# Kernel tuning notes

Hardware: AMD Instinct MI355X
Metric: run time of the kernel (lower is better)

## Reference

```python
import jax, jax.numpy as jnp
import numpy as np

N = 30000          # num nodes
E = 480000         # num edges (avg degree 16)
IN = 1024          # in_channels
OUT = 128          # out_channels
MAX_DEG = 48       # static cap on per-node in-degree (incl. self-loop); Poisson(16) max over 30k nodes << 48


def setup_inputs() -> dict:
    key = jax.random.key(0)
    k1, k2, k3 = jax.random.split(key, 3)
    x = jax.random.normal(k1, (N, IN), dtype=jnp.float32)
    edge_index = jax.random.randint(k2, (2, E), 0, N, dtype=jnp.int64)
    W = jax.random.normal(k3, (IN, OUT), dtype=jnp.float32) * (1.0 / np.sqrt(IN))
    b = jnp.zeros((OUT,), dtype=jnp.float32)
    return {"x": x, "edge_index": edge_index, "W": W, "b": b}


def _median_conv(x, edge_index, W, b):
    # linear transform first (as in the torch module)
    h = x @ W                                   # [N, OUT]
    n = x.shape[0]
    # add self-loops
    loop = jnp.arange(n, dtype=edge_index.dtype)
    row = jnp.concatenate([edge_index[0], loop])  # source nodes
    col = jnp.concatenate([edge_index[1], loop])  # destination nodes
    # sort edges by destination (jnp.argsort is stable)
    order = jnp.argsort(col)
    row_s = row[order]
    col_s = col[order]
    x_j = h[row_s]                              # [Etot, OUT] gathered neighbor features
    # per-destination degree and within-segment slot index
    ones = jnp.ones_like(col_s)
    deg = jax.ops.segment_sum(ones, col_s, num_segments=n)      # [N]
    start = jnp.cumsum(deg) - deg                                # segment start offsets
    slot = jnp.arange(col_s.shape[0], dtype=col_s.dtype) - start[col_s]
    # padded dense batch [N, MAX_DEG, OUT]; pads = +inf so they sort to the end
    dense = jnp.full((n, MAX_DEG, h.shape[1]), jnp.inf, dtype=h.dtype)
    dense = dense.at[col_s, slot].set(x_j)
    sdense = jnp.sort(dense, axis=1)
    # torch.median returns the LOWER median: sorted index (deg-1)//2
    med_idx = jnp.maximum(deg - 1, 0) // 2                       # [N]
    out = jnp.take_along_axis(sdense, med_idx[:, None, None], axis=1)[:, 0, :]
    # zero-degree nodes would yield +inf; self-loops guarantee deg>=1, but guard anyway
    out = jnp.where((deg > 0)[:, None], out, jnp.zeros_like(out))
    return out + b


def reference(x, edge_index, W, b):
    return _median_conv(x, edge_index, W, b)
```

## Files before the change

kernel.cpp:

```cpp
#include <hip/hip_runtime.h>
#include <hip/hip_bf16.h>

#define N_NODES 30000
#define N_EDGES 480000
#define IN_CH   1024
#define OUT_CH  128
#define MAX_DEG 48

#define BM 64
#define BK 64
#define NSTEP (IN_CH / BK)

typedef float   f32x4  __attribute__((ext_vector_type(4)));
typedef __bf16  bf16x8 __attribute__((ext_vector_type(8)));
typedef unsigned short ushort8 __attribute__((ext_vector_type(8)));
typedef unsigned int   uint4v  __attribute__((ext_vector_type(4)));

__device__ __forceinline__ unsigned short f2bf(float f) {
  unsigned int u = __builtin_bit_cast(unsigned int, f);
  u += 0x7fffu + ((u >> 16) & 1u);
  return (unsigned short)(u >> 16);
}

__device__ __forceinline__ unsigned int cvt_pk(float lo, float hi) {
  unsigned int r;
  asm("v_cvt_pk_bf16_f32 %0, %1, %2" : "=v"(r) : "v"(lo), "v"(hi));
  return r;
}

__device__ __forceinline__ void gload_lds16(const void* g, void* l) {
  __builtin_amdgcn_global_load_lds(
      (const __attribute__((address_space(1))) void*)g,
      (__attribute__((address_space(3))) void*)l, 16, 0, 0);
}

__global__ __launch_bounds__(256) void convert_W(const float* __restrict__ W,
                                                 unsigned short* __restrict__ Wt) {
  int idx = blockIdx.x * 256 + threadIdx.x;
  int n = idx >> 10;
  int k = idx & 1023;
  Wt[idx] = f2bf(W[k * OUT_CH + n]);
}

__global__ __launch_bounds__(256) void build_adj(const int* __restrict__ ei,
                                                 int* __restrict__ deg,
                                                 int* __restrict__ adj) {
  int i = blockIdx.x * blockDim.x + threadIdx.x;
  const int total = N_EDGES + N_NODES;
  if (i >= total) return;
  int src, dst;
  if (i < N_EDGES) { src = ei[i]; dst = ei[N_EDGES + i]; }
  else             { src = i - N_EDGES; dst = src; }
  int slot = atomicAdd(&deg[dst], 1);
  if (slot < MAX_DEG) adj[dst * MAX_DEG + slot] = src;
}

__global__ __launch_bounds__(256) void gemm_h(const float* __restrict__ x,
                                              const unsigned short* __restrict__ Wt,
                                              const float* __restrict__ bias,
                                              float* __restrict__ h) {
  __shared__ char smem[2 * 32768];
  const int tid  = threadIdx.x;
  const int wv   = tid >> 6;
  const int lane = tid & 63;
  const int l16  = lane & 15;
  const int g4   = lane >> 4;
  const int m0   = blockIdx.x * BM;

  f32x4 acc[4][2];
#pragma unroll
  for (int rf = 0; rf < 4; ++rf)
#pragma unroll
    for (int cf = 0; cf < 2; ++cf) acc[rf][cf] = (f32x4){0.f, 0.f, 0.f, 0.f};

  auto stage = [&](int buf, int st) {
    const int k0 = st * BK;
    char* sA = smem + buf * 32768;
    char* sB = sA + 16384;
#pragma unroll
    for (int j = 0; j < 4; ++j) {
      const int blk = wv * 4 + j;
      const int rowA = blk * 4 + (lane >> 4);
      int rg = m0 + rowA;
      if (rg > N_NODES - 1) rg = N_NODES - 1;
      const float* srcA = x + (size_t)rg * IN_CH + k0
                        + (((lane & 15) ^ (rowA & 15)) << 2);
      gload_lds16(srcA, sA + blk * 1024 + lane * 16);
      const int c = blk * 8 + (lane >> 3);
      const unsigned short* srcB = Wt + (size_t)c * IN_CH + k0
                                 + (((lane & 7) ^ (c & 7)) << 3);
      gload_lds16(srcB, sB + blk * 1024 + lane * 16);
    }
  };

  auto compute = [&](int buf) {
    const char* sA = smem + buf * 32768;
    const char* sB = sA + 16384;
#pragma unroll
    for (int ks = 0; ks < 2; ++ks) {
      bf16x8 bfr[2];
#pragma unroll
      for (int cf = 0; cf < 2; ++cf) {
        const int c = wv * 32 + cf * 16 + l16;
        const int slot = (ks * 4 + g4) ^ (c & 7);
        bfr[cf] = *(const bf16x8*)(sB + c * 128 + slot * 16);
      }
#pragma unroll
      for (int rf = 0; rf < 4; ++rf) {
        const int row = rf * 16 + l16;
        const int q0 = ((ks * 8 + g4 * 2) ^ (row & 15)) << 4;
        const int q1 = ((ks * 8 + g4 * 2 + 1) ^ (row & 15)) << 4;
        f32x4 a0 = *(const f32x4*)(sA + row * 256 + q0);
        f32x4 a1 = *(const f32x4*)(sA + row * 256 + q1);
        uint4v aw;
        aw[0] = cvt_pk(a0[0], a0[1]);
        aw[1] = cvt_pk(a0[2], a0[3]);
        aw[2] = cvt_pk(a1[0], a1[1]);
        aw[3] = cvt_pk(a1[2], a1[3]);
        bf16x8 av = __builtin_bit_cast(bf16x8, aw);
        acc[rf][0] = __builtin_amdgcn_mfma_f32_16x16x32_bf16(av, bfr[0], acc[rf][0], 0, 0, 0);
        acc[rf][1] = __builtin_amdgcn_mfma_f32_16x16x32_bf16(av, bfr[1], acc[rf][1], 0, 0, 0);
      }
    }
  };

  stage(0, 0);
  __syncthreads();
  int cur = 0;
  for (int st = 0; st < NSTEP - 1; ++st) {
    stage(cur ^ 1, st + 1);
    compute(cur);
    __syncthreads();
    cur ^= 1;
  }
  compute(cur);

  const int crow0 = m0 + g4 * 4;
#pragma unroll
  for (int cf = 0; cf < 2; ++cf) {
    const int col = wv * 32 + cf * 16 + l16;
    const float bv = bias[col];
#pragma unroll
    for (int rf = 0; rf < 4; ++rf) {
#pragma unroll
      for (int i = 0; i < 4; ++i) {
        int r = crow0 + rf * 16 + i;
        if (r < N_NODES) h[(size_t)r * OUT_CH + col] = acc[rf][cf][i] + bv;
      }
    }
  }
}

template <int NS>
__device__ __forceinline__ void batcher_sort(float (&a)[NS]) {
#pragma unroll
  for (int p = 1; p < NS; p <<= 1) {
#pragma unroll
    for (int k = p; k >= 1; k >>= 1) {
#pragma unroll
      for (int j = k % p; j + k < NS; j += 2 * k) {
#pragma unroll
        for (int i = 0; i < k; ++i) {
          if (i + j + k < NS) {
            if ((i + j) / (2 * p) == (i + j + k) / (2 * p)) {
              float lo = fminf(a[i + j], a[i + j + k]);
              float hi = fmaxf(a[i + j], a[i + j + k]);
              a[i + j] = lo;
              a[i + j + k] = hi;
            }
          }
        }
      }
    }
  }
}

template <int NS>
__device__ __forceinline__ float med_n(const float* __restrict__ h,
                                       const int* nbrs, int d, int m, int ch) {
  float a[NS];
#pragma unroll
  for (int j = 0; j < NS; ++j) {
    if (j < d) a[j] = h[(size_t)nbrs[j] * OUT_CH + ch];
    else       a[j] = 1e30f;
  }
  batcher_sort<NS>(a);
  float med = a[0];
#pragma unroll
  for (int j = 1; j < NS; ++j) med = (j == m) ? a[j] : med;
  return med;
}

__global__ __launch_bounds__(128) void median_kernel(const float* __restrict__ h,
                                                     const int* __restrict__ adj,
                                                     const int* __restrict__ deg,
                                                     float* __restrict__ out) {
  __shared__ int nbrs[64];
  const int node = blockIdx.x;
  const int ch   = threadIdx.x;
  int d = deg[node];
  if (d > MAX_DEG) d = MAX_DEG;
  if (ch < 64) nbrs[ch] = (ch < d && ch < MAX_DEG) ? adj[node * MAX_DEG + ch] : 0;
  __syncthreads();
  const int m = (d - 1) >> 1;

  float med;
  if (d <= 8)       med = med_n<8>(h, nbrs, d, m, ch);
  else if (d <= 16) med = med_n<16>(h, nbrs, d, m, ch);
  else if (d <= 32) med = med_n<32>(h, nbrs, d, m, ch);
  else              med = med_n<64>(h, nbrs, d, m, ch);

  out[(size_t)node * OUT_CH + ch] = med;
}

extern "C" void kernel_launch(void* const* d_in, const int* in_sizes, int n_in,
                              void* d_out, int out_size, void* d_ws, size_t ws_size,
                              hipStream_t stream) {
  const float* x  = (const float*)d_in[0];
  const int*   ei = (const int*)d_in[1];
  const float* W  = (const float*)d_in[2];
  const float* b  = (const float*)d_in[3];
  float* out = (float*)d_out;

  char* ws = (char*)d_ws;
  float*          h   = (float*)ws;
  unsigned short* Wt  = (unsigned short*)(ws + 15360000);
  int*            deg = (int*)(ws + 15360000 + 262144);
  int*            adj = (int*)(ws + 15360000 + 262144 + 120000);

  hipMemsetAsync(deg, 0, N_NODES * sizeof(int), stream);
  convert_W<<<dim3(131072 / 256), dim3(256), 0, stream>>>(W, Wt);
  build_adj<<<dim3((N_EDGES + N_NODES + 255) / 256), dim3(256), 0, stream>>>(ei, deg, adj);
  gemm_h<<<dim3((N_NODES + BM - 1) / BM), dim3(256), 0, stream>>>(x, Wt, b, h);
  median_kernel<<<dim3(N_NODES), dim3(128), 0, stream>>>(h, adj, deg, out);
}
```

Baseline: 273.9 us.

## Store h as fp16 and sort two channels per lane with packed f16 min/max

```diff
diff --git a/kernel.cpp b/kernel.cpp
--- a/kernel.cpp
+++ b/kernel.cpp
@@ -7,11 +7,12 @@
 #define OUT_CH  128
 #define MAX_DEG 48
 
-#define BM 64
+#define BM 32
 #define BK 64
 #define NSTEP (IN_CH / BK)
 
 typedef float   f32x4  __attribute__((ext_vector_type(4)));
+typedef float   f32x2  __attribute__((ext_vector_type(2)));
 typedef __bf16  bf16x8 __attribute__((ext_vector_type(8)));
 typedef unsigned short ushort8 __attribute__((ext_vector_type(8)));
 typedef unsigned int   uint4v  __attribute__((ext_vector_type(4)));
@@ -28,6 +29,20 @@
   return r;
 }
 
+__device__ __forceinline__ unsigned pk_min(unsigned a, unsigned b) {
+  unsigned r; asm("v_pk_min_f16 %0, %1, %2" : "=v"(r) : "v"(a), "v"(b)); return r;
+}
+__device__ __forceinline__ unsigned pk_max(unsigned a, unsigned b) {
+  unsigned r; asm("v_pk_max_f16 %0, %1, %2" : "=v"(r) : "v"(a), "v"(b)); return r;
+}
+__device__ __forceinline__ float f16_to_f32(unsigned u16) {
+  float f; asm("v_cvt_f32_f16 %0, %1" : "=v"(f) : "v"(u16)); return f;
+}
+__device__ __forceinline__ unsigned short f32_to_f16(float f) {
+  unsigned r; asm("v_cvt_f16_f32 %0, %1" : "=v"(r) : "v"(f));
+  return (unsigned short)(r & 0xffffu);
+}
+
 __device__ __forceinline__ void gload_lds16(const void* g, void* l) {
   __builtin_amdgcn_global_load_lds(
       (const __attribute__((address_space(1))) void*)g,
@@ -35,11 +50,26 @@
 }
 
 __global__ __launch_bounds__(256) void convert_W(const float* __restrict__ W,
-                                                 unsigned short* __restrict__ Wt) {
-  int idx = blockIdx.x * 256 + threadIdx.x;
-  int n = idx >> 10;
-  int k = idx & 1023;
-  Wt[idx] = f2bf(W[k * OUT_CH + n]);
+                                                 unsigned short* __restrict__ Wtt) {
+  __shared__ float tile[64][132];
+  const int tid = threadIdx.x;
+  const int k0  = blockIdx.x * 64;
+#pragma unroll
+  for (int it = 0; it < 32; ++it) {
+    int id = it * 256 + tid;
+    int kk = id >> 7, n = id & 127;
+    tile[kk][n] = W[(size_t)(k0 + kk) * OUT_CH + n];
+  }
+  __syncthreads();
+#pragma unroll
+  for (int it = 0; it < 4; ++it) {
+    int id8 = it * 256 + tid;
+    int kc = id8 >> 7, n = id8 & 127;
+    ushort8 v;
+#pragma unroll
+    for (int kd = 0; kd < 8; ++kd) v[kd] = f2bf(tile[kc * 8 + kd][n]);
+    *(ushort8*)(Wtt + (size_t)k0 * 128 + id8 * 8) = v;
+  }
 }
 
 __global__ __launch_bounds__(256) void build_adj(const int* __restrict__ ei,
@@ -56,10 +86,10 @@
 }
 
 __global__ __launch_bounds__(256) void gemm_h(const float* __restrict__ x,
-                                              const unsigned short* __restrict__ Wt,
+                                              const unsigned short* __restrict__ Wtt,
                                               const float* __restrict__ bias,
-                                              float* __restrict__ h) {
-  __shared__ char smem[2 * 32768];
+                                              unsigned short* __restrict__ h16) {
+  __shared__ float sA[2][BM * BK];
   const int tid  = threadIdx.x;
   const int wv   = tid >> 6;
   const int lane = tid & 63;
@@ -67,92 +97,96 @@
   const int g4   = lane >> 4;
   const int m0   = blockIdx.x * BM;
 
-  f32x4 acc[4][2];
-#pragma unroll
-  for (int rf = 0; rf < 4; ++rf)
+  f32x4 acc[2][2];
+#pragma unroll
+  for (int rf = 0; rf < 2; ++rf)
 #pragma unroll
     for (int cf = 0; cf < 2; ++cf) acc[rf][cf] = (f32x4){0.f, 0.f, 0.f, 0.f};
 
-  auto stage = [&](int buf, int st) {
-    const int k0 = st * BK;
-    char* sA = smem + buf * 32768;
-    char* sB = sA + 16384;
-#pragma unroll
-    for (int j = 0; j < 4; ++j) {
-      const int blk = wv * 4 + j;
-      const int rowA = blk * 4 + (lane >> 4);
+  auto stageA = [&](int p, int st) {
+#pragma unroll
+    for (int j = 0; j < 2; ++j) {
+      const int blk  = wv * 2 + j;
+      const int rowA = blk * 4 + g4;
       int rg = m0 + rowA;
       if (rg > N_NODES - 1) rg = N_NODES - 1;
-      const float* srcA = x + (size_t)rg * IN_CH + k0
-                        + (((lane & 15) ^ (rowA & 15)) << 2);
-      gload_lds16(srcA, sA + blk * 1024 + lane * 16);
-      const int c = blk * 8 + (lane >> 3);
-      const unsigned short* srcB = Wt + (size_t)c * IN_CH + k0
-                                 + (((lane & 7) ^ (c & 7)) << 3);
-      gload_lds16(srcB, sB + blk * 1024 + lane * 16);
+      const float* src = x + (size_t)rg * IN_CH + st * BK
+                       + ((l16 ^ (rowA & 15)) << 2);
+      gload_lds16(src, (char*)&sA[p][0] + blk * 1024 + lane * 16);
     }
   };
-
-  auto compute = [&](int buf) {
-    const char* sA = smem + buf * 32768;
-    const char* sB = sA + 16384;
-#pragma unroll
-    for (int ks = 0; ks < 2; ++ks) {
-      bf16x8 bfr[2];
-#pragma unroll
-      for (int cf = 0; cf < 2; ++cf) {
-        const int c = wv * 32 + cf * 16 + l16;
-        const int slot = (ks * 4 + g4) ^ (c & 7);
-        bfr[cf] = *(const bf16x8*)(sB + c * 128 + slot * 16);
-      }
-#pragma unroll
-      for (int rf = 0; rf < 4; ++rf) {
+  auto loadB = [&](bf16x8 (&B)[2][2], int st) {
+#pragma unroll
+    for (int cf = 0; cf < 2; ++cf)
+#pragma unroll
+      for (int ks = 0; ks < 2; ++ks) {
+        const int col = wv * 32 + cf * 16 + l16;
+        const int kc  = st * 8 + ks * 4 + g4;
+        B[cf][ks] = *(const bf16x8*)(Wtt + ((size_t)kc * 128 + col) * 8);
+      }
+  };
+  auto compute = [&](int p, bf16x8 (&B)[2][2]) {
+    const char* base = (const char*)&sA[p][0];
+#pragma unroll
+    for (int ks = 0; ks < 2; ++ks)
+#pragma unroll
+      for (int rf = 0; rf < 2; ++rf) {
         const int row = rf * 16 + l16;
-        const int q0 = ((ks * 8 + g4 * 2) ^ (row & 15)) << 4;
-        const int q1 = ((ks * 8 + g4 * 2 + 1) ^ (row & 15)) << 4;
-        f32x4 a0 = *(const f32x4*)(sA + row * 256 + q0);
-        f32x4 a1 = *(const f32x4*)(sA + row * 256 + q1);
+        const int s0  = ks * 8 + g4 * 2;
+        f32x4 a0 = *(const f32x4*)(base + row * 256 + (((s0    ) ^ (row & 15)) << 4));
+        f32x4 a1 = *(const f32x4*)(base + row * 256 + (((s0 + 1) ^ (row & 15)) << 4));
         uint4v aw;
-        aw[0] = cvt_pk(a0[0], a0[1]);
-        aw[1] = cvt_pk(a0[2], a0[3]);
-        aw[2] = cvt_pk(a1[0], a1[1]);
-        aw[3] = cvt_pk(a1[2], a1[3]);
+        aw[0] = cvt_pk(a0[0], a0[1]); aw[1] = cvt_pk(a0[2], a0[3]);
+        aw[2] = cvt_pk(a1[0], a1[1]); aw[3] = cvt_pk(a1[2], a1[3]);
         bf16x8 av = __builtin_bit_cast(bf16x8, aw);
-        acc[rf][0] = __builtin_amdgcn_mfma_f32_16x16x32_bf16(av, bfr[0], acc[rf][0], 0, 0, 0);
-        acc[rf][1] = __builtin_amdgcn_mfma_f32_16x16x32_bf16(av, bfr[1], acc[rf][1], 0, 0, 0);
-      }
-    }
+        acc[rf][0] = __builtin_amdgcn_mfma_f32_16x16x32_bf16(av, B[0][ks], acc[rf][0], 0, 0, 0);
+        acc[rf][1] = __builtin_amdgcn_mfma_f32_16x16x32_bf16(av, B[1][ks], acc[rf][1], 0, 0, 0);
+      }
   };
 
-  stage(0, 0);
-  __syncthreads();
-  int cur = 0;
-  for (int st = 0; st < NSTEP - 1; ++st) {
-    stage(cur ^ 1, st + 1);
-    compute(cur);
-    __syncthreads();
-    cur ^= 1;
-  }
-  compute(cur);
-
-  const int crow0 = m0 + g4 * 4;
+#define WAIT6_BAR() asm volatile("s_waitcnt vmcnt(6)\ns_barrier" ::: "memory")
+#define WAIT0_BAR() asm volatile("s_waitcnt vmcnt(0)\ns_barrier" ::: "memory")
+#define BAR()       asm volatile("s_barrier" ::: "memory")
+
+  bf16x8 B0[2][2], B1[2][2];
+  stageA(0, 0); loadB(B0, 0);
+  stageA(1, 1); loadB(B1, 1);
+#pragma unroll
+  for (int s2 = 0; s2 < 7; ++s2) {
+    const int se = s2 * 2;
+    WAIT6_BAR();
+    compute(0, B0);
+    BAR();
+    stageA(0, se + 2); loadB(B0, se + 2);
+    WAIT6_BAR();
+    compute(1, B1);
+    BAR();
+    stageA(1, se + 3); loadB(B1, se + 3);
+  }
+  WAIT6_BAR();  compute(0, B0);
+  WAIT0_BAR();  compute(1, B1);
+
+  const int r0 = m0 + g4 * 4;
 #pragma unroll
   for (int cf = 0; cf < 2; ++cf) {
     const int col = wv * 32 + cf * 16 + l16;
     const float bv = bias[col];
 #pragma unroll
-    for (int rf = 0; rf < 4; ++rf) {
+    for (int rf = 0; rf < 2; ++rf)
 #pragma unroll
       for (int i = 0; i < 4; ++i) {
-        int r = crow0 + rf * 16 + i;
-        if (r < N_NODES) h[(size_t)r * OUT_CH + col] = acc[rf][cf][i] + bv;
-      }
-    }
-  }
+        int r = r0 + rf * 16 + i;
+        if (r < N_NODES)
+          h16[(size_t)r * OUT_CH + col] = f32_to_f16(acc[rf][cf][i] + bv);
+      }
+  }
+#undef WAIT6_BAR
+#undef WAIT0_BAR
+#undef BAR
 }
 
 template <int NS>
-__device__ __forceinline__ void batcher_sort(float (&a)[NS]) {
+__device__ __forceinline__ void sortnet(unsigned (&a)[NS]) {
 #pragma unroll
   for (int p = 1; p < NS; p <<= 1) {
 #pragma unroll
@@ -163,8 +197,8 @@
         for (int i = 0; i < k; ++i) {
           if (i + j + k < NS) {
             if ((i + j) / (2 * p) == (i + j + k) / (2 * p)) {
-              float lo = fminf(a[i + j], a[i + j + k]);
-              float hi = fmaxf(a[i + j], a[i + j + k]);
+              unsigned lo = pk_min(a[i + j], a[i + j + k]);
+              unsigned hi = pk_max(a[i + j], a[i + j + k]);
               a[i + j] = lo;
               a[i + j + k] = hi;
             }
@@ -176,41 +210,46 @@
 }
 
 template <int NS>
-__device__ __forceinline__ float med_n(const float* __restrict__ h,
-                                       const int* nbrs, int d, int m, int ch) {
-  float a[NS];
+__device__ __forceinline__ unsigned med_n(const unsigned short* __restrict__ h16,
+                                          const int* nb, int d, int m, int lane) {
+  unsigned a[NS];
 #pragma unroll
   for (int j = 0; j < NS; ++j) {
-    if (j < d) a[j] = h[(size_t)nbrs[j] * OUT_CH + ch];
-    else       a[j] = 1e30f;
-  }
-  batcher_sort<NS>(a);
-  float med = a[0];
+    unsigned v = *(const unsigned*)(h16 + (size_t)nb[j] * OUT_CH + lane * 2);
+    a[j] = (j < d) ? v : 0x7C007C00u;
+  }
+  sortnet<NS>(a);
+  unsigned med = a[0];
 #pragma unroll
   for (int j = 1; j < NS; ++j) med = (j == m) ? a[j] : med;
   return med;
 }
 
-__global__ __launch_bounds__(128) void median_kernel(const float* __restrict__ h,
+__global__ __launch_bounds__(256) void median_kernel(const unsigned short* __restrict__ h16,
                                                      const int* __restrict__ adj,
                                                      const int* __restrict__ deg,
                                                      float* __restrict__ out) {
-  __shared__ int nbrs[64];
-  const int node = blockIdx.x;
-  const int ch   = threadIdx.x;
+  __shared__ int nb[4][MAX_DEG];
+  const int wv   = threadIdx.x >> 6;
+  const int lane = threadIdx.x & 63;
+  const int node = blockIdx.x * 4 + wv;
+
   int d = deg[node];
   if (d > MAX_DEG) d = MAX_DEG;
-  if (ch < 64) nbrs[ch] = (ch < d && ch < MAX_DEG) ? adj[node * MAX_DEG + ch] : 0;
-  __syncthreads();
+  if (lane < MAX_DEG)
+    nb[wv][lane] = (lane < d) ? adj[node * MAX_DEG + lane] : node;
   const int m = (d - 1) >> 1;
 
-  float med;
-  if (d <= 8)       med = med_n<8>(h, nbrs, d, m, ch);
-  else if (d <= 16) med = med_n<16>(h, nbrs, d, m, ch);
-  else if (d <= 32) med = med_n<32>(h, nbrs, d, m, ch);
-  else              med = med_n<64>(h, nbrs, d, m, ch);
-
-  out[(size_t)node * OUT_CH + ch] = med;
+  unsigned med;
+  if (d <= 16)      med = med_n<16>(h16, nb[wv], d, m, lane);
+  else if (d <= 24) med = med_n<24>(h16, nb[wv], d, m, lane);
+  else if (d <= 32) med = med_n<32>(h16, nb[wv], d, m, lane);
+  else              med = med_n<48>(h16, nb[wv], d, m, lane);
+
+  f32x2 o;
+  o[0] = f16_to_f32(med & 0xffffu);
+  o[1] = f16_to_f32(med >> 16);
+  *(f32x2*)(out + (size_t)node * OUT_CH + lane * 2) = o;
 }
 
 extern "C" void kernel_launch(void* const* d_in, const int* in_sizes, int n_in,
@@ -223,14 +262,14 @@
   float* out = (float*)d_out;
 
   char* ws = (char*)d_ws;
-  float*          h   = (float*)ws;
-  unsigned short* Wt  = (unsigned short*)(ws + 15360000);
-  int*            deg = (int*)(ws + 15360000 + 262144);
-  int*            adj = (int*)(ws + 15360000 + 262144 + 120000);
-
-  hipMemsetAsync(deg, 0, N_NODES * sizeof(int), stream);
-  convert_W<<<dim3(131072 / 256), dim3(256), 0, stream>>>(W, Wt);
+  unsigned short* h16 = (unsigned short*)ws;
+  unsigned short* Wtt = (unsigned short*)(ws + 7680000);
+  int*            deg = (int*)(ws + 7680000 + 262144);
+  int*            adj = (int*)(ws + 7680000 + 262144 + 120000);
+
+  (void)hipMemsetAsync(deg, 0, N_NODES * sizeof(int), stream);
+  convert_W<<<dim3(IN_CH / 64), dim3(256), 0, stream>>>(W, Wtt);
   build_adj<<<dim3((N_EDGES + N_NODES + 255) / 256), dim3(256), 0, stream>>>(ei, deg, adj);
-  gemm_h<<<dim3((N_NODES + BM - 1) / BM), dim3(256), 0, stream>>>(x, Wt, b, h);
-  median_kernel<<<dim3(N_NODES), dim3(128), 0, stream>>>(h, adj, deg, out);
-}
+  gemm_h<<<dim3((N_NODES + BM - 1) / BM), dim3(256), 0, stream>>>(x, Wtt, b, h16);
+  median_kernel<<<dim3(N_NODES / 4), dim3(256), 0, stream>>>(h16, adj, deg, out);
+}
```

New measurement: 251.4 us. 8.2% less time.
